# Performance work log

Measured on AMD Instinct MI355X. Metric: run time of the kernel, lower is better.

Reference implementation:

```python
import jax, jax.numpy as jnp
import numpy as np

N_NODES = 100000
N_EDGES = 1600000
THRESHOLD = 10.0
EPS = 1e-5


def setup_inputs() -> dict:
    key = jax.random.key(0)
    ks = jax.random.split(key, 8)
    x = jax.random.normal(ks[0], (N_NODES, 128), dtype=jnp.float32)
    edge_index = jax.random.randint(ks[1], (2, N_EDGES), 0, N_NODES, dtype=jnp.int64)
    # distances strictly in (0, threshold]
    edge_attr = jax.random.uniform(ks[2], (N_EDGES, 1), dtype=jnp.float32,
                                   minval=EPS, maxval=THRESHOLD)
    W1 = jax.random.normal(ks[3], (1, 128), dtype=jnp.float32) * 0.1
    b1 = jax.random.normal(ks[4], (128,), dtype=jnp.float32) * 0.1
    W2 = jax.random.normal(ks[5], (128, 54), dtype=jnp.float32) * 0.1
    b2 = jax.random.normal(ks[6], (54,), dtype=jnp.float32) * 0.1
    return {"x": x, "edge_index": edge_index, "edge_attr": edge_attr,
            "W1": W1, "b1": b1, "W2": W2, "b2": b2}


def reference(x, edge_index, edge_attr, W1, b1, W2, b2):
    # --- one-hot distance bucketize (vectorized replacement of the per-edge
    # Python loop with .item() in the original) ---
    dist = edge_attr[:, 0]                                   # [E]
    interval = THRESHOLD / 10.0
    bucket = jnp.clip((dist / interval).astype(jnp.int32), 0, 9)  # int() truncation, index 10 -> 9
    one_hot = jax.nn.one_hot(bucket, 10, dtype=edge_attr.dtype)   # [E, 10]

    # --- edge MLP: Linear(1->H) -> ReLU -> Linear(H->O) -> ReLU ---
    h = jax.nn.relu(edge_attr @ W1 + b1)                     # [E, 128]
    mlp_out = jax.nn.relu(h @ W2 + b2)                       # [E, 54]

    w = jnp.concatenate([one_hot, mlp_out], axis=1)          # [E, 64]

    # --- scatter-sum by source node, gather back, normalize ---
    src = edge_index[0]                                      # [E]
    d = jax.ops.segment_sum(w, src, num_segments=N_NODES)    # [N, 64]
    dtilde = d[src]                                          # [E, 64]
    # safe divide: where dtilde==0, w is also 0 (one-hot/ReLU sums), define 0/0 := 0
    nz = dtilde != 0
    wtilde = jnp.where(nz, w / jnp.where(nz, dtilde, 1.0), 0.0)
    return wtilde
```

## Files before the change

### kernel.cpp

```cpp
#include <hip/hip_runtime.h>

#define N_NODES   100000
#define N_EDGES   1600000
#define COLS      64
#define HID       128
#define OUT2      54
#define NSEG_MAX  129
#define LUT_N     4096
#define CAP       64
#define MAXS      12

#define OFF_COUNTS  0ull
#define OFF_SORTED  400000ull
#define OFF_ALPHA   26000000ull
#define OFF_BETA    26033024ull
#define OFF_BG      26066048ull
#define OFF_META    26066560ull
#define OFF_LUT     26066576ull

__global__ __launch_bounds__(256) void build_kernel(
    const float* __restrict__ W1, const float* __restrict__ b1,
    float* __restrict__ Bg, int* __restrict__ meta,
    unsigned short* __restrict__ LUT)
{
    __shared__ float tval[HID];
    __shared__ float Bs[HID];
    __shared__ int mcnt;
    const int tid = threadIdx.x;
    if (tid == 0) mcnt = 0;
    __syncthreads();
    bool valid = false; float tj = 0.f;
    if (tid < HID) {
        const float w = W1[tid], b = b1[tid];
        tj = -b / w;
        valid = (w != 0.f) && (tj > 0.f) && (tj < 10.f);
        tval[tid] = valid ? tj : 1e30f;
    }
    __syncthreads();
    if (valid) {
        int r = 0;
        for (int i = 0; i < HID; ++i) {
            const float ti = tval[i];
            r += (ti < tj || (ti == tj && i < tid)) ? 1 : 0;
        }
        Bs[r] = tj;
        atomicAdd(&mcnt, 1);
    }
    __syncthreads();
    const int m = mcnt;
    if (tid == 0) meta[0] = m;
    if (tid < m) Bg[tid] = Bs[tid];
    for (int b = tid; b < LUT_N; b += 256) {
        const float tb = (float)b * (10.0f / LUT_N);
        int s = 0;
        for (int i = 0; i < m; ++i) s += (Bs[i] <= tb) ? 1 : 0;
        LUT[b] = (unsigned short)s;
    }
}

__global__ __launch_bounds__(64) void table_kernel(
    const float* __restrict__ W1, const float* __restrict__ b1,
    const float* __restrict__ W2, const float* __restrict__ b2,
    const float* __restrict__ Bg, const int* __restrict__ meta,
    float* __restrict__ alpha, float* __restrict__ beta)
{
    const int m = meta[0];
    const int s = blockIdx.x;
    if (s > m) return;
    const float L = (s == 0) ? 0.0f : Bg[s - 1];
    const float R = (s == m) ? 10.0f : Bg[s];
    const float mid = 0.5f * (L + R);
    const int col = threadIdx.x;
    float a = 0.f, bb = 0.f;
    if (col >= 10) {
        const int k = col - 10;
        a = b2[k];
        for (int j = 0; j < HID; ++j) {
            const float w1j = W1[j], b1j = b1[j];
            if (fmaf(w1j, mid, b1j) > 0.f) {
                const float w2 = W2[j * OUT2 + k];
                a  = fmaf(w2, b1j, a);
                bb = fmaf(w2, w1j, bb);
            }
        }
    }
    alpha[s * COLS + col] = a;
    beta [s * COLS + col] = bb;
}

__global__ __launch_bounds__(256) void scatter_kernel(
    const int*   __restrict__ edge_index,
    int*  __restrict__ counts,
    int*  __restrict__ sorted_eid)
{
    const int e = blockIdx.x * 256 + threadIdx.x;
    const int s = edge_index[e];
    const int pos = atomicAdd(&counts[s], 1);
    if (pos < CAP)
        sorted_eid[(s << 6) + pos] = e;
}

__device__ __forceinline__ int seg_of(float t, int m,
    const float* __restrict__ Bg, const unsigned short* __restrict__ LUT)
{
    int li = (int)(t * ((float)LUT_N / 10.0f));
    li = li < 0 ? 0 : (li > (LUT_N - 1) ? (LUT_N - 1) : li);
    int s = LUT[li];
    while (s < m && Bg[s] <= t) ++s;
    while (s > 0 && Bg[s - 1] > t) --s;
    return s;
}

__device__ __forceinline__ float4 pwl_quad(float t, int bkt, int c, int seg,
    const float* __restrict__ alpha, const float* __restrict__ beta)
{
    const float4 av = ((const float4*)(alpha + seg * COLS))[c];
    const float4 bv = ((const float4*)(beta  + seg * COLS))[c];
    const int j0 = c * 4;
    float4 w;
    w.x = ((bkt == j0 + 0) ? 1.f : 0.f) + fmaxf(fmaf(bv.x, t, av.x), 0.f);
    w.y = ((bkt == j0 + 1) ? 1.f : 0.f) + fmaxf(fmaf(bv.y, t, av.y), 0.f);
    w.z = ((bkt == j0 + 2) ? 1.f : 0.f) + fmaxf(fmaf(bv.z, t, av.z), 0.f);
    w.w = ((bkt == j0 + 3) ? 1.f : 0.f) + fmaxf(fmaf(bv.w, t, av.w), 0.f);
    return w;
}

__global__ __launch_bounds__(256) void dsum_norm_kernel(
    const float* __restrict__ edge_attr,
    const int*  __restrict__ counts,
    const int*  __restrict__ sorted_eid,
    const float* __restrict__ alpha,
    const float* __restrict__ beta,
    const float* __restrict__ Bg,
    const int*   __restrict__ meta,
    const unsigned short* __restrict__ LUT,
    float*       __restrict__ out)
{
    const int node = blockIdx.x * 4 + (threadIdx.x >> 6);
    const int lane = threadIdx.x & 63;
    const int c    = lane & 15;
    const int g    = lane >> 4;
    const int m    = meta[0];
    int n = counts[node];
    n = n > CAP ? CAP : n;
    const int* __restrict__ bucket = sorted_eid + (node << 6);

    float4 acc = make_float4(0.f, 0.f, 0.f, 0.f);
    float4 stash[MAXS];
    int    eids[MAXS];

#pragma unroll
    for (int si = 0; si < MAXS; ++si) {
        const int idx = si * 4 + g;
        float4 wv = make_float4(0.f, 0.f, 0.f, 0.f);
        int eid = 0;
        if (idx < n) {
            eid = bucket[idx];
            const float t = edge_attr[eid];
            int bkt = (int)t; bkt = bkt < 0 ? 0 : (bkt > 9 ? 9 : bkt);
            const int s = seg_of(t, m, Bg, LUT);
            wv = pwl_quad(t, bkt, c, s, alpha, beta);
            acc.x += wv.x; acc.y += wv.y; acc.z += wv.z; acc.w += wv.w;
        }
        eids[si] = eid; stash[si] = wv;
    }
    for (int i = MAXS * 4; i < n; i += 4) {
        const int idx = i + g;
        if (idx < n) {
            const int eid = bucket[idx];
            const float t = edge_attr[eid];
            int bkt = (int)t; bkt = bkt < 0 ? 0 : (bkt > 9 ? 9 : bkt);
            const int s = seg_of(t, m, Bg, LUT);
            const float4 wv = pwl_quad(t, bkt, c, s, alpha, beta);
            acc.x += wv.x; acc.y += wv.y; acc.z += wv.z; acc.w += wv.w;
        }
    }

#pragma unroll
    for (int mm = 16; mm <= 32; mm <<= 1) {
        acc.x += __shfl_xor(acc.x, mm, 64);
        acc.y += __shfl_xor(acc.y, mm, 64);
        acc.z += __shfl_xor(acc.z, mm, 64);
        acc.w += __shfl_xor(acc.w, mm, 64);
    }

    float4 inv;
    inv.x = (acc.x != 0.f) ? __builtin_amdgcn_rcpf(acc.x) : 0.f;
    inv.y = (acc.y != 0.f) ? __builtin_amdgcn_rcpf(acc.y) : 0.f;
    inv.z = (acc.z != 0.f) ? __builtin_amdgcn_rcpf(acc.z) : 0.f;
    inv.w = (acc.w != 0.f) ? __builtin_amdgcn_rcpf(acc.w) : 0.f;

#pragma unroll
    for (int si = 0; si < MAXS; ++si) {
        const int idx = si * 4 + g;
        if (idx < n) {
            float4 wv = stash[si];
            wv.x *= inv.x; wv.y *= inv.y; wv.z *= inv.z; wv.w *= inv.w;
            ((float4*)(out + (long long)eids[si] * COLS))[c] = wv;
        }
    }
    for (int i = MAXS * 4; i < n; i += 4) {
        const int idx = i + g;
        if (idx < n) {
            const int eid = bucket[idx];
            const float t = edge_attr[eid];
            int bkt = (int)t; bkt = bkt < 0 ? 0 : (bkt > 9 ? 9 : bkt);
            const int s = seg_of(t, m, Bg, LUT);
            float4 wv = pwl_quad(t, bkt, c, s, alpha, beta);
            wv.x *= inv.x; wv.y *= inv.y; wv.z *= inv.z; wv.w *= inv.w;
            ((float4*)(out + (long long)eid * COLS))[c] = wv;
        }
    }
}

extern "C" void kernel_launch(void* const* d_in, const int* in_sizes, int n_in,
                              void* d_out, int out_size, void* d_ws, size_t ws_size,
                              hipStream_t stream) {
    const int*   edge_index = (const int*)d_in[1];
    const float* edge_attr  = (const float*)d_in[2];
    const float* W1         = (const float*)d_in[3];
    const float* b1         = (const float*)d_in[4];
    const float* W2         = (const float*)d_in[5];
    const float* b2         = (const float*)d_in[6];
    float* out = (float*)d_out;

    char* ws = (char*)d_ws;
    int*   counts     = (int*)  (ws + OFF_COUNTS);
    int*   sorted_eid = (int*)  (ws + OFF_SORTED);
    float* alpha      = (float*)(ws + OFF_ALPHA);
    float* beta       = (float*)(ws + OFF_BETA);
    float* Bg         = (float*)(ws + OFF_BG);
    int*   meta       = (int*)  (ws + OFF_META);
    unsigned short* LUT = (unsigned short*)(ws + OFF_LUT);

    hipMemsetAsync(counts, 0, (size_t)N_NODES * sizeof(int), stream);

    build_kernel<<<1, 256, 0, stream>>>(W1, b1, Bg, meta, LUT);

    table_kernel<<<NSEG_MAX, 64, 0, stream>>>(W1, b1, W2, b2, Bg, meta, alpha, beta);

    scatter_kernel<<<N_EDGES / 256, 256, 0, stream>>>(
        edge_index, counts, sorted_eid);

    dsum_norm_kernel<<<N_NODES / 4, 256, 0, stream>>>(
        edge_attr, counts, sorted_eid, alpha, beta, Bg, meta, LUT, out);
}
```

Measured before the change: 802.0 us.

## Batch edge loads up front, use nontemporal output stores, and set occupancy hint

The normalize kernel now loads all stashed edge ids and their distances in unconditional batches, clamping indices to the last valid edge, so the gathers can be in flight at once instead of being serialized behind per-iteration branches. Invalid slots are masked by multiplying with zero rather than branching. Output writes use nontemporal stores to avoid polluting cache with the large streamed result, and launch bounds request three blocks per SM. Nodes with zero edges exit early. The costs are extra redundant loads for padded slots and higher register pressure from the batched arrays.

Result: slower. 828.7 us (+3.3%).

```diff
diff --git a/kernel.cpp b/kernel.cpp
--- a/kernel.cpp
+++ b/kernel.cpp
@@ -9,6 +9,8 @@
 #define LUT_N     4096
 #define CAP       64
 #define MAXS      12
+
+typedef float f32x4 __attribute__((ext_vector_type(4)));
 
 #define OFF_COUNTS  0ull
 #define OFF_SORTED  400000ull
@@ -125,7 +127,13 @@
     return w;
 }
 
-__global__ __launch_bounds__(256) void dsum_norm_kernel(
+__device__ __forceinline__ void nt_store4(float* p, float4 v)
+{
+    f32x4 x; x.x = v.x; x.y = v.y; x.z = v.z; x.w = v.w;
+    __builtin_nontemporal_store(x, (f32x4*)p);
+}
+
+__global__ __launch_bounds__(256, 3) void dsum_norm_kernel(
     const float* __restrict__ edge_attr,
     const int*  __restrict__ counts,
     const int*  __restrict__ sorted_eid,
@@ -143,26 +151,33 @@
     const int m    = meta[0];
     int n = counts[node];
     n = n > CAP ? CAP : n;
+    if (n == 0) return;
     const int* __restrict__ bucket = sorted_eid + (node << 6);
+    const int nm1 = n - 1;
+
+    int eidr[MAXS];
+#pragma unroll
+    for (int si = 0; si < MAXS; ++si) {
+        const int idx = si * 4 + g;
+        eidr[si] = bucket[idx < nm1 ? idx : nm1];
+    }
+    float tr[MAXS];
+#pragma unroll
+    for (int si = 0; si < MAXS; ++si) tr[si] = edge_attr[eidr[si]];
 
     float4 acc = make_float4(0.f, 0.f, 0.f, 0.f);
     float4 stash[MAXS];
-    int    eids[MAXS];
-
 #pragma unroll
     for (int si = 0; si < MAXS; ++si) {
         const int idx = si * 4 + g;
-        float4 wv = make_float4(0.f, 0.f, 0.f, 0.f);
-        int eid = 0;
-        if (idx < n) {
-            eid = bucket[idx];
-            const float t = edge_attr[eid];
-            int bkt = (int)t; bkt = bkt < 0 ? 0 : (bkt > 9 ? 9 : bkt);
-            const int s = seg_of(t, m, Bg, LUT);
-            wv = pwl_quad(t, bkt, c, s, alpha, beta);
-            acc.x += wv.x; acc.y += wv.y; acc.z += wv.z; acc.w += wv.w;
-        }
-        eids[si] = eid; stash[si] = wv;
+        const float t = tr[si];
+        int bkt = (int)t; bkt = bkt < 0 ? 0 : (bkt > 9 ? 9 : bkt);
+        const int s = seg_of(t, m, Bg, LUT);
+        float4 wv = pwl_quad(t, bkt, c, s, alpha, beta);
+        const float msk = (idx < n) ? 1.0f : 0.0f;
+        wv.x *= msk; wv.y *= msk; wv.z *= msk; wv.w *= msk;
+        stash[si] = wv;
+        acc.x += wv.x; acc.y += wv.y; acc.z += wv.z; acc.w += wv.w;
     }
     for (int i = MAXS * 4; i < n; i += 4) {
         const int idx = i + g;
@@ -196,7 +211,7 @@
         if (idx < n) {
             float4 wv = stash[si];
             wv.x *= inv.x; wv.y *= inv.y; wv.z *= inv.z; wv.w *= inv.w;
-            ((float4*)(out + (long long)eids[si] * COLS))[c] = wv;
+            nt_store4(out + (long long)eidr[si] * COLS + c * 4, wv);
         }
     }
     for (int i = MAXS * 4; i < n; i += 4) {
@@ -208,7 +223,7 @@
             const int s = seg_of(t, m, Bg, LUT);
             float4 wv = pwl_quad(t, bkt, c, s, alpha, beta);
             wv.x *= inv.x; wv.y *= inv.y; wv.z *= inv.z; wv.w *= inv.w;
-            ((float4*)(out + (long long)eid * COLS))[c] = wv;
+            nt_store4(out + (long long)eid * COLS + c * 4, wv);
         }
     }
 }
@@ -233,7 +248,7 @@
     int*   meta       = (int*)  (ws + OFF_META);
     unsigned short* LUT = (unsigned short*)(ws + OFF_LUT);
 
-    hipMemsetAsync(counts, 0, (size_t)N_NODES * sizeof(int), stream);
+    (void)hipMemsetAsync(counts, 0, (size_t)N_NODES * sizeof(int), stream);
 
     build_kernel<<<1, 256, 0, stream>>>(W1, b1, Bg, meta, LUT);
 
```
